# Kernel tuning notes

Measured on AMD Instinct MI355X. Metric: run time of the kernel, lower is better.

## Reference

```python
import jax, jax.numpy as jnp
import numpy as np
from jax import lax

DIM = 192
HEADS = 8
EPS = 1e-5


def setup_inputs() -> dict:
    key = jax.random.key(0)
    ks = jax.random.split(key, 8)
    B, C, H, W = 1, DIM, 64, 64
    x = jax.random.normal(ks[0], (B, C, H, W), dtype=jnp.float32)
    gamma = jnp.ones((C,), dtype=jnp.float32)
    beta = jnp.zeros((C,), dtype=jnp.float32)
    w_qkv = jax.random.normal(ks[1], (3 * C, C), dtype=jnp.float32) * (1.0 / np.sqrt(C))
    # depthwise 3x3 conv: (out_ch=3C, in_ch/groups=1, 3, 3), bias present (Conv2d default)
    w_dw = jax.random.normal(ks[2], (3 * C, 1, 3, 3), dtype=jnp.float32) * (1.0 / 3.0)
    b_dw = jax.random.normal(ks[3], (3 * C,), dtype=jnp.float32) * 0.01
    w_proj = jax.random.normal(ks[4], (C, C), dtype=jnp.float32) * (1.0 / np.sqrt(C))
    temperature = jnp.ones((HEADS, 1, 1), dtype=jnp.float32)
    return {"x": x, "gamma": gamma, "beta": beta, "w_qkv": w_qkv,
            "w_dw": w_dw, "b_dw": b_dw, "w_proj": w_proj,
            "temperature": temperature}


def _mdta(x, gamma, beta, w_qkv, w_dw, b_dw, w_proj, temperature):
    B, C, H, W = x.shape
    heads = HEADS
    d = C // heads
    N = H * W
    # LayerNorm over channel dim (applied on NHWC permute in torch)
    mean = jnp.mean(x, axis=1, keepdims=True)
    var = jnp.var(x, axis=1, keepdims=True)
    x_ln = (x - mean) * lax.rsqrt(var + EPS)
    x_ln = x_ln * gamma[None, :, None, None] + beta[None, :, None, None]
    # 1x1 conv (no bias): [B,3C,H,W]
    qkv = jnp.einsum('oc,bchw->bohw', w_qkv, x_ln)
    # depthwise 3x3 conv, padding=1, groups=3C
    qkv = lax.conv_general_dilated(
        qkv, w_dw, window_strides=(1, 1), padding=((1, 1), (1, 1)),
        dimension_numbers=('NCHW', 'OIHW', 'NCHW'),
        feature_group_count=3 * C)
    qkv = qkv + b_dw[None, :, None, None]
    q, k, v = jnp.split(qkv, 3, axis=1)
    q = q.reshape(B, heads, d, N)
    k = k.reshape(B, heads, d, N)
    v = v.reshape(B, heads, d, N)
    # attn[b,h,n,m] = sum_d q[b,h,d,n] k[b,h,d,m], scaled by learnable temperature
    attn = jnp.einsum('bhdn,bhdm->bhnm', q, k) * temperature  # (heads,1,1) broadcasts
    attn = jax.nn.softmax(attn, axis=-1)
    # out[b,h,d,n] = sum_m attn[b,h,n,m] v[b,h,d,m]
    out = jnp.einsum('bhnm,bhdm->bhdn', attn, v)
    out = out.reshape(B, C, H, W)
    out = jnp.einsum('oc,bchw->bohw', w_proj, out)
    return out + x


def reference(x, gamma, beta, w_qkv, w_dw, b_dw, w_proj, temperature):
    return _mdta(x, gamma, beta, w_qkv, w_dw, b_dw, w_proj, temperature)
```

## Files before the change

### kernel.cpp

```cpp
#include <hip/hip_runtime.h>
#include <hip/hip_bf16.h>


typedef __bf16 bf16;
typedef __bf16 bf16x2 __attribute__((ext_vector_type(2)));
typedef __bf16 bf16x4 __attribute__((ext_vector_type(4)));
typedef __bf16 bf16x8 __attribute__((ext_vector_type(8)));
typedef float f32x4 __attribute__((ext_vector_type(4)));

#define C_DIM 192
#define N_PIX 4096
#define HEADS 8
#define DHEAD 24
#define DPAD 32
#define C3 576
#define NSPLIT 8

__device__ inline float fast_exp2(float x) {
#if __has_builtin(__builtin_amdgcn_exp2f)
    return __builtin_amdgcn_exp2f(x);
#else
    return exp2f(x);
#endif
}

__device__ inline f32x4 mfma16(bf16x8 a, bf16x8 b, f32x4 c) {
    return __builtin_amdgcn_mfma_f32_16x16x32_bf16(a, b, c, 0, 0, 0);
}

__global__ __launch_bounds__(256) void ln_qkv(const float* __restrict__ x,
                                              const float* __restrict__ gamma,
                                              const float* __restrict__ beta,
                                              const float* __restrict__ wqkv,
                                              bf16* __restrict__ qkvb,
                                              float* __restrict__ maxk2) {
    __shared__ __align__(16) bf16 Bt[64 * 200];
    __shared__ float gs[C_DIM], bs[C_DIM];
    const int K = C_DIM;
    int n0 = blockIdx.x * 64;
    int m0 = blockIdx.y * 64;
    int t = threadIdx.x;
    if (t < C_DIM) { gs[t] = gamma[t]; bs[t] = beta[t]; }
    if (blockIdx.x == 0 && blockIdx.y == 0 && t < 8) maxk2[t] = 0.0f;
    __syncthreads();

    int lane = t & 63, wave = t >> 6;
    {
        int pl = wave * 16 + (lane & 15);
        int seg = lane >> 4;
        int p = n0 + pl;
        float v[48];
        float s = 0.f, ss = 0.f;
        for (int j = 0; j < 48; ++j) {
            float f = x[(seg * 48 + j) * N_PIX + p];
            v[j] = f; s += f; ss += f * f;
        }
        s += __shfl_xor(s, 16, 64); s += __shfl_xor(s, 32, 64);
        ss += __shfl_xor(ss, 16, 64); ss += __shfl_xor(ss, 32, 64);
        float mean = s * (1.0f / C_DIM);
        float var = ss * (1.0f / C_DIM) - mean * mean;
        float rstd = rsqrtf(var + 1e-5f);
        bf16* dst = Bt + pl * 200 + seg * 48;
        for (int g = 0; g < 6; ++g) {
            bf16x8 w;
            for (int j = 0; j < 8; ++j) {
                int c = seg * 48 + g * 8 + j;
                w[j] = (bf16)((v[g * 8 + j] - mean) * rstd * gs[c] + bs[c]);
            }
            *(bf16x8*)(dst + g * 8) = w;
        }
    }
    __syncthreads();

    int l16 = lane & 15, quad = lane >> 4;
    int wm = (wave >> 1) * 32, wn = (wave & 1) * 32;
    f32x4 acc[2][2] = {};
    for (int kk = 0; kk < K; kk += 32) {
        const f32x4* ar0 = (const f32x4*)(wqkv + (m0 + wm + l16) * K + kk + quad * 8);
        const f32x4* ar1 = (const f32x4*)(wqkv + (m0 + wm + 16 + l16) * K + kk + quad * 8);
        f32x4 w0a = ar0[0], w0b = ar0[1];
        f32x4 w1a = ar1[0], w1b = ar1[1];
        bf16x8 a0, a1;
        for (int j = 0; j < 4; ++j) {
            a0[j] = (bf16)w0a[j]; a0[4 + j] = (bf16)w0b[j];
            a1[j] = (bf16)w1a[j]; a1[4 + j] = (bf16)w1b[j];
        }
        bf16x8 b0 = *(const bf16x8*)(Bt + (wn + l16) * 200 + kk + quad * 8);
        bf16x8 b1 = *(const bf16x8*)(Bt + (wn + 16 + l16) * 200 + kk + quad * 8);
        acc[0][0] = mfma16(a0, b0, acc[0][0]);
        acc[0][1] = mfma16(a0, b1, acc[0][1]);
        acc[1][0] = mfma16(a1, b0, acc[1][0]);
        acc[1][1] = mfma16(a1, b1, acc[1][1]);
    }
    for (int i = 0; i < 2; ++i)
        for (int j = 0; j < 2; ++j)
            for (int r = 0; r < 4; ++r) {
                int row = m0 + wm + i * 16 + quad * 4 + r;
                int col = n0 + wn + j * 16 + l16;
                qkvb[(size_t)row * N_PIX + col] = (bf16)acc[i][j][r];
            }
}

__global__ __launch_bounds__(256) void dwconv(const bf16* __restrict__ qkv,
                                              const float* __restrict__ wdw,
                                              const float* __restrict__ bdw,
                                              bf16* __restrict__ qt,
                                              bf16* __restrict__ kt,
                                              bf16* __restrict__ vl,
                                              float* __restrict__ maxk2) {
    __shared__ float k2s[24][64];
    __shared__ bf16 stg[64 * DPAD];
    int bx = blockIdx.x;
    int part = bx >> 9;
    int h = (bx >> 6) & 7;
    int y = bx & 63;
    int t = threadIdx.x;
    int ch_local = t >> 3;
    int seg = t & 7;
    int px0 = seg * 8;
    bool active = ch_local < 24;

    float acc[8];
    if (active) {
        int ch = part * C_DIM + h * DHEAD + ch_local;
        const bf16* in = qkv + (size_t)ch * N_PIX;
        float w[9];
        for (int i = 0; i < 9; ++i) w[i] = wdw[ch * 9 + i];
        float bias = bdw[ch];
        float rowv[3][10];
        for (int r = 0; r < 3; ++r) {
            int yy = y + r - 1;
            if (yy >= 0 && yy < 64) {
                bf16x8 v8 = *(const bf16x8*)(in + yy * 64 + px0);
                for (int j = 0; j < 8; ++j) rowv[r][j + 1] = (float)v8[j];
                rowv[r][0] = (seg > 0) ? (float)in[yy * 64 + px0 - 1] : 0.f;
                rowv[r][9] = (seg < 7) ? (float)in[yy * 64 + px0 + 8] : 0.f;
            } else {
                for (int j = 0; j < 10; ++j) rowv[r][j] = 0.f;
            }
        }
        for (int j = 0; j < 8; ++j) {
            float a = bias;
            for (int r = 0; r < 3; ++r)
                a += w[r * 3 + 0] * rowv[r][j] + w[r * 3 + 1] * rowv[r][j + 1]
                   + w[r * 3 + 2] * rowv[r][j + 2];
            acc[j] = a;
        }
    }

    if (part == 2) {
        if (active) {
            bf16x8 v8;
            for (int j = 0; j < 8; ++j) v8[j] = (bf16)acc[j];
            *(bf16x8*)(vl + ((size_t)(h * DPAD + ch_local)) * N_PIX + y * 64 + px0) = v8;
        } else {
            int i = t - 192;
            int dd = 24 + (i >> 3);
            int s2 = i & 7;
            bf16 val = (bf16)((dd == 24) ? 1.0f : 0.0f);
            bf16x8 v8;
            for (int j = 0; j < 8; ++j) v8[j] = val;
            *(bf16x8*)(vl + ((size_t)(h * DPAD + dd)) * N_PIX + y * 64 + s2 * 8) = v8;
        }
    } else {
        if (active) {
            for (int j = 0; j < 8; ++j)
                stg[(px0 + j) * DPAD + ch_local] = (bf16)acc[j];
        } else {
            int i = t - 192;
            bf16x8 z;
            for (int j = 0; j < 8; ++j) z[j] = (bf16)0.0f;
            *(bf16x8*)(stg + i * DPAD + 24) = z;
        }
        if (part == 1 && active)
            for (int j = 0; j < 8; ++j) k2s[ch_local][px0 + j] = acc[j] * acc[j];
        __syncthreads();
        bf16* dst = (part == 0 ? qt : kt) + ((size_t)h * N_PIX + y * 64) * DPAD;
        *(bf16x8*)(dst + t * 8) = *(const bf16x8*)(stg + t * 8);
        if (part == 1 && t < 64) {
            float s = 0.f;
            for (int c = 0; c < 24; ++c) s += k2s[c][t];
            for (int off = 1; off < 64; off <<= 1)
                s = fmaxf(s, __shfl_xor(s, off, 64));
            if (t == 0) atomicMax((unsigned int*)(maxk2 + h), __float_as_uint(s));
        }
    }
}

__global__ __launch_bounds__(256, 4) void flash_attn(const bf16* __restrict__ qt,
                                                     const bf16* __restrict__ kt,
                                                     const bf16* __restrict__ vl,
                                                     const float* __restrict__ temp,
                                                     const float* __restrict__ maxk2,
                                                     bf16* __restrict__ opart,
                                                     bf16* __restrict__ lpart) {
    __shared__ __align__(16) bf16 Plds[16 * 1024];

    int tid = threadIdx.x;
    int wave = tid >> 6, lane = tid & 63;
    int l16 = lane & 15, quad = lane >> 4;
    int head = blockIdx.x & 7;
    int qb = (blockIdx.x >> 3) & 15;
    int split = blockIdx.x >> 7;
    int nbase = qb * 256 + wave * 64;
    float tl = temp[head] * 1.44269504f;

    const bf16* qrow = qt + ((size_t)head * N_PIX + nbase) * DPAD;
    bf16x8 aq[4];
    for (int f = 0; f < 4; ++f)
        aq[f] = *(const bf16x8*)(qrow + (size_t)(f * 16 + l16) * DPAD + quad * 8);

    float mk2 = maxk2[head];
    float Bb[4];
    for (int f = 0; f < 4; ++f) {
        float q2 = 0.f;
        for (int j = 0; j < 8; ++j) { float v = (float)aq[f][j]; q2 += v * v; }
        q2 += __shfl_xor(q2, 16, 64);
        q2 += __shfl_xor(q2, 32, 64);
        Bb[f] = fabsf(tl) * sqrtf(q2 * mk2) + 1.0f;
    }

    const bf16* kbase = kt + (size_t)head * N_PIX * DPAD;
    const bf16* vbase = vl + (size_t)head * DPAD * N_PIX;
    bf16* pw = Plds + wave * 4096;

    f32x4 o0[4] = {}, o1[4] = {};

    const int NITER = 64 / NSPLIT;
    int mbase = split * NITER * 64;

    bf16x8 ak[4];
    for (int mt = 0; mt < 4; ++mt)
        ak[mt] = *(const bf16x8*)(kbase + (size_t)(mbase + mt * 16 + l16) * DPAD + quad * 8);

    #pragma unroll 2
    for (int it = 0; it < NITER; ++it) {
        int m0 = mbase + it * 64;
        bf16x8 av0 = *(const bf16x8*)(vbase + (size_t)l16 * N_PIX + m0 + quad * 8);
        bf16x8 av1 = *(const bf16x8*)(vbase + (size_t)(16 + l16) * N_PIX + m0 + quad * 8);
        bf16x8 av2 = *(const bf16x8*)(vbase + (size_t)l16 * N_PIX + m0 + 32 + quad * 8);
        bf16x8 av3 = *(const bf16x8*)(vbase + (size_t)(16 + l16) * N_PIX + m0 + 32 + quad * 8);
        bf16x8 akn[4];
        if (it + 1 < NITER) {
            int m1 = m0 + 64;
            for (int mt = 0; mt < 4; ++mt)
                akn[mt] = *(const bf16x8*)(kbase + (size_t)(m1 + mt * 16 + l16) * DPAD + quad * 8);
        }

        for (int f = 0; f < 4; ++f) {
            bf16* pwf = pw + f * 1024;
            __builtin_amdgcn_s_setprio(1);
            f32x4 z = {0.f, 0.f, 0.f, 0.f};
            f32x4 st[4];
            for (int mt = 0; mt < 4; ++mt) st[mt] = mfma16(ak[mt], aq[f], z);
            for (int mt = 0; mt < 4; ++mt) {
                bf16x4 pk;
                for (int r = 0; r < 4; ++r)
                    pk[r] = (bf16)fast_exp2(__builtin_fmaf(st[mt][r], tl, -Bb[f]));
                int chunk = mt * 2 + (quad >> 1);
                *(bf16x4*)(pwf + (chunk * 16 + l16) * 8 + (quad & 1) * 4) = pk;
            }
            bf16x8 ap0 = *(const bf16x8*)(pwf + (quad * 16 + l16) * 8);
            bf16x8 ap1 = *(const bf16x8*)(pwf + ((4 + quad) * 16 + l16) * 8);
            o0[f] = mfma16(av0, ap0, o0[f]);
            o1[f] = mfma16(av1, ap0, o1[f]);
            o0[f] = mfma16(av2, ap1, o0[f]);
            o1[f] = mfma16(av3, ap1, o1[f]);
            __builtin_amdgcn_s_setprio(0);
        }
        if (it + 1 < NITER)
            for (int mt = 0; mt < 4; ++mt) ak[mt] = akn[mt];
    }

    for (int f = 0; f < 4; ++f) {
        int n = nbase + f * 16 + l16;
        size_t rowo = ((size_t)(split * 8 + head) * N_PIX + n) * 24;
        bf16x4 w0;
        for (int r = 0; r < 4; ++r) w0[r] = (bf16)o0[f][r];
        *(bf16x4*)(opart + rowo + quad * 4) = w0;
        if (quad < 2) {
            bf16x4 w1;
            for (int r = 0; r < 4; ++r) w1[r] = (bf16)o1[f][r];
            *(bf16x4*)(opart + rowo + 16 + quad * 4) = w1;
        }
        if (quad == 2)
            lpart[(size_t)(split * 8 + head) * N_PIX + n] = (bf16)o1[f][0];
    }
}

__global__ __launch_bounds__(256) void gemm_proj(const float* __restrict__ wproj,
                                                 const bf16* __restrict__ opart,
                                                 const bf16* __restrict__ lpart,
                                                 float* __restrict__ outf,
                                                 const float* __restrict__ resid) {
    __shared__ __align__(16) bf16 Bld[32 * 200];
    const int K = C_DIM;
    int n0 = blockIdx.x * 32;
    int m0 = blockIdx.y * 64;
    int t = threadIdx.x;
    {
        int h = t >> 5, nl = t & 31;
        int n = n0 + nl;
        float acc[24];
        for (int j = 0; j < 24; ++j) acc[j] = 0.f;
        float l = 0.f;
        for (int s = 0; s < NSPLIT; ++s) {
            const bf16* row = opart + ((size_t)(s * 8 + h) * N_PIX + n) * 24;
            bf16x8 a = *(const bf16x8*)(row);
            bf16x8 b = *(const bf16x8*)(row + 8);
            bf16x8 c = *(const bf16x8*)(row + 16);
            for (int j = 0; j < 8; ++j) {
                acc[j] += (float)a[j];
                acc[8 + j] += (float)b[j];
                acc[16 + j] += (float)c[j];
            }
            l += (float)lpart[(size_t)(s * 8 + h) * N_PIX + n];
        }
        float inv = 1.0f / l;
        bf16* dst = Bld + nl * 200 + h * 24;
        for (int g = 0; g < 3; ++g) {
            bf16x8 w;
            for (int j = 0; j < 8; ++j) w[j] = (bf16)(acc[g * 8 + j] * inv);
            *(bf16x8*)(dst + g * 8) = w;
        }
    }
    __syncthreads();
    int wave = t >> 6, lane = t & 63;
    int l16 = lane & 15, quad = lane >> 4;
    int mrow = m0 + wave * 16;
    float rv[8];
    for (int j = 0; j < 2; ++j)
        for (int r = 0; r < 4; ++r)
            rv[j * 4 + r] = resid[(size_t)(mrow + quad * 4 + r) * N_PIX + n0 + j * 16 + l16];
    f32x4 acc2[2] = {};
    for (int kk = 0; kk < K; kk += 32) {
        const f32x4* ar = (const f32x4*)(wproj + (mrow + l16) * K + kk + quad * 8);
        f32x4 wa = ar[0], wb = ar[1];
        bf16x8 a;
        for (int j = 0; j < 4; ++j) { a[j] = (bf16)wa[j]; a[4 + j] = (bf16)wb[j]; }
        bf16x8 b0 = *(const bf16x8*)(Bld + l16 * 200 + kk + quad * 8);
        bf16x8 b1 = *(const bf16x8*)(Bld + (16 + l16) * 200 + kk + quad * 8);
        acc2[0] = mfma16(a, b0, acc2[0]);
        acc2[1] = mfma16(a, b1, acc2[1]);
    }
    for (int j = 0; j < 2; ++j)
        for (int r = 0; r < 4; ++r) {
            int row = mrow + quad * 4 + r;
            int col = n0 + j * 16 + l16;
            outf[(size_t)row * N_PIX + col] = acc2[j][r] + rv[j * 4 + r];
        }
}

extern "C" void kernel_launch(void* const* d_in, const int* in_sizes, int n_in,
                              void* d_out, int out_size, void* d_ws, size_t ws_size,
                              hipStream_t stream) {
    const float* x     = (const float*)d_in[0];
    const float* gamma = (const float*)d_in[1];
    const float* beta  = (const float*)d_in[2];
    const float* wqkv  = (const float*)d_in[3];
    const float* wdw   = (const float*)d_in[4];
    const float* bdw   = (const float*)d_in[5];
    const float* wproj = (const float*)d_in[6];
    const float* temp  = (const float*)d_in[7];
    float* out = (float*)d_out;

    char* ws = (char*)d_ws;
    bf16* qkv     = (bf16*)(ws + 0);
    bf16* qt      = (bf16*)(ws + 4718592);
    bf16* kt      = (bf16*)(ws + 6815744);
    bf16* vl      = (bf16*)(ws + 8912896);
    bf16* opart   = (bf16*)(ws + 11010048);
    bf16* lpart   = (bf16*)(ws + 23592960);
    float* maxk2  = (float*)(ws + 24117248);

    ln_qkv<<<dim3(64, 9), 256, 0, stream>>>(x, gamma, beta, wqkv, qkv, maxk2);
    dwconv<<<1536, 256, 0, stream>>>(qkv, wdw, bdw, qt, kt, vl, maxk2);
    flash_attn<<<NSPLIT * 128, 256, 0, stream>>>(qt, kt, vl, temp, maxk2, opart, lpart);
    gemm_proj<<<dim3(128, 3), 256, 0, stream>>>(wproj, opart, lpart, out, x);
}
```

Measured before the change: 131.1 us.

## Shrink flash-attention tiles to 32 queries per wave and 32-key steps

Each wave in the attention kernel now handles 32 query rows instead of 64 and walks the keys in 32-wide steps. Grid doubles to 2048 blocks and shared memory per block drops to a quarter, which should allow more resident blocks and more parallelism. The explicit register prefetch of the next K tile is removed and the loop is no longer unrolled. Each K/V load is now reused across fewer queries, so global/L2 traffic for K and V roughly doubles, and memory latency is less hidden.

```diff
diff --git a/kernel.cpp b/kernel.cpp
--- a/kernel.cpp
+++ b/kernel.cpp
@@ -194,25 +194,25 @@
                                                      const float* __restrict__ maxk2,
                                                      bf16* __restrict__ opart,
                                                      bf16* __restrict__ lpart) {
-    __shared__ __align__(16) bf16 Plds[16 * 1024];
+    __shared__ __align__(16) bf16 Plds[4 * 1024];
 
     int tid = threadIdx.x;
     int wave = tid >> 6, lane = tid & 63;
     int l16 = lane & 15, quad = lane >> 4;
     int head = blockIdx.x & 7;
-    int qb = (blockIdx.x >> 3) & 15;
-    int split = blockIdx.x >> 7;
-    int nbase = qb * 256 + wave * 64;
+    int qb = (blockIdx.x >> 3) & 31;
+    int split = blockIdx.x >> 8;
+    int nbase = qb * 128 + wave * 32;
     float tl = temp[head] * 1.44269504f;
 
     const bf16* qrow = qt + ((size_t)head * N_PIX + nbase) * DPAD;
-    bf16x8 aq[4];
-    for (int f = 0; f < 4; ++f)
+    bf16x8 aq[2];
+    for (int f = 0; f < 2; ++f)
         aq[f] = *(const bf16x8*)(qrow + (size_t)(f * 16 + l16) * DPAD + quad * 8);
 
     float mk2 = maxk2[head];
-    float Bb[4];
-    for (int f = 0; f < 4; ++f) {
+    float Bb[2];
+    for (int f = 0; f < 2; ++f) {
         float q2 = 0.f;
         for (int j = 0; j < 8; ++j) { float v = (float)aq[f][j]; q2 += v * v; }
         q2 += __shfl_xor(q2, 16, 64);
@@ -222,57 +222,44 @@
 
     const bf16* kbase = kt + (size_t)head * N_PIX * DPAD;
     const bf16* vbase = vl + (size_t)head * DPAD * N_PIX;
-    bf16* pw = Plds + wave * 4096;
-
-    f32x4 o0[4] = {}, o1[4] = {};
-
-    const int NITER = 64 / NSPLIT;
-    int mbase = split * NITER * 64;
-
-    bf16x8 ak[4];
-    for (int mt = 0; mt < 4; ++mt)
-        ak[mt] = *(const bf16x8*)(kbase + (size_t)(mbase + mt * 16 + l16) * DPAD + quad * 8);
-
-    #pragma unroll 2
+    bf16* pw = Plds + wave * 1024;
+
+    f32x4 o0[2] = {}, o1[2] = {};
+
+    const int NITER = N_PIX / NSPLIT / 32;
+    int mbase = split * NITER * 32;
+
+    #pragma unroll 1
     for (int it = 0; it < NITER; ++it) {
-        int m0 = mbase + it * 64;
-        bf16x8 av0 = *(const bf16x8*)(vbase + (size_t)l16 * N_PIX + m0 + quad * 8);
-        bf16x8 av1 = *(const bf16x8*)(vbase + (size_t)(16 + l16) * N_PIX + m0 + quad * 8);
-        bf16x8 av2 = *(const bf16x8*)(vbase + (size_t)l16 * N_PIX + m0 + 32 + quad * 8);
-        bf16x8 av3 = *(const bf16x8*)(vbase + (size_t)(16 + l16) * N_PIX + m0 + 32 + quad * 8);
-        bf16x8 akn[4];
-        if (it + 1 < NITER) {
-            int m1 = m0 + 64;
-            for (int mt = 0; mt < 4; ++mt)
-                akn[mt] = *(const bf16x8*)(kbase + (size_t)(m1 + mt * 16 + l16) * DPAD + quad * 8);
-        }
-
-        for (int f = 0; f < 4; ++f) {
-            bf16* pwf = pw + f * 1024;
+        int m0 = mbase + it * 32;
+        bf16x8 ak0 = *(const bf16x8*)(kbase + (size_t)(m0 + l16) * DPAD + quad * 8);
+        bf16x8 ak1 = *(const bf16x8*)(kbase + (size_t)(m0 + 16 + l16) * DPAD + quad * 8);
+        bf16x8 avl = *(const bf16x8*)(vbase + (size_t)l16 * N_PIX + m0 + quad * 8);
+        bf16x8 avh = *(const bf16x8*)(vbase + (size_t)(16 + l16) * N_PIX + m0 + quad * 8);
+
+        for (int f = 0; f < 2; ++f) {
+            bf16* pwf = pw + f * 512;
+            f32x4 z = {0.f, 0.f, 0.f, 0.f};
             __builtin_amdgcn_s_setprio(1);
-            f32x4 z = {0.f, 0.f, 0.f, 0.f};
-            f32x4 st[4];
-            for (int mt = 0; mt < 4; ++mt) st[mt] = mfma16(ak[mt], aq[f], z);
-            for (int mt = 0; mt < 4; ++mt) {
-                bf16x4 pk;
-                for (int r = 0; r < 4; ++r)
-                    pk[r] = (bf16)fast_exp2(__builtin_fmaf(st[mt][r], tl, -Bb[f]));
-                int chunk = mt * 2 + (quad >> 1);
-                *(bf16x4*)(pwf + (chunk * 16 + l16) * 8 + (quad & 1) * 4) = pk;
-            }
-            bf16x8 ap0 = *(const bf16x8*)(pwf + (quad * 16 + l16) * 8);
-            bf16x8 ap1 = *(const bf16x8*)(pwf + ((4 + quad) * 16 + l16) * 8);
-            o0[f] = mfma16(av0, ap0, o0[f]);
-            o1[f] = mfma16(av1, ap0, o1[f]);
-            o0[f] = mfma16(av2, ap1, o0[f]);
-            o1[f] = mfma16(av3, ap1, o1[f]);
+            f32x4 st0 = mfma16(ak0, aq[f], z);
+            f32x4 st1 = mfma16(ak1, aq[f], z);
             __builtin_amdgcn_s_setprio(0);
-        }
-        if (it + 1 < NITER)
-            for (int mt = 0; mt < 4; ++mt) ak[mt] = akn[mt];
-    }
-
-    for (int f = 0; f < 4; ++f) {
+            bf16x4 pk0, pk1;
+            for (int r = 0; r < 4; ++r) {
+                pk0[r] = (bf16)fast_exp2(__builtin_fmaf(st0[r], tl, -Bb[f]));
+                pk1[r] = (bf16)fast_exp2(__builtin_fmaf(st1[r], tl, -Bb[f]));
+            }
+            *(bf16x4*)(pwf + (((quad >> 1)) * 16 + l16) * 8 + (quad & 1) * 4) = pk0;
+            *(bf16x4*)(pwf + ((2 + (quad >> 1)) * 16 + l16) * 8 + (quad & 1) * 4) = pk1;
+            bf16x8 ap = *(const bf16x8*)(pwf + (quad * 16 + l16) * 8);
+            __builtin_amdgcn_s_setprio(1);
+            o0[f] = mfma16(avl, ap, o0[f]);
+            o1[f] = mfma16(avh, ap, o1[f]);
+            __builtin_amdgcn_s_setprio(0);
+        }
+    }
+
+    for (int f = 0; f < 2; ++f) {
         int n = nbase + f * 16 + l16;
         size_t rowo = ((size_t)(split * 8 + head) * N_PIX + n) * 24;
         bf16x4 w0;
@@ -375,6 +362,6 @@
 
     ln_qkv<<<dim3(64, 9), 256, 0, stream>>>(x, gamma, beta, wqkv, qkv, maxk2);
     dwconv<<<1536, 256, 0, stream>>>(qkv, wdw, bdw, qt, kt, vl, maxk2);
-    flash_attn<<<NSPLIT * 128, 256, 0, stream>>>(qt, kt, vl, temp, maxk2, opart, lpart);
+    flash_attn<<<2048, 256, 0, stream>>>(qt, kt, vl, temp, maxk2, opart, lpart);
     gemm_proj<<<dim3(128, 3), 256, 0, stream>>>(wproj, opart, lpart, out, x);
 }
```

Result: slower. 151.8 us (+15.8%).
